# Optimization experiments

Hardware: AMD Instinct MI355X
Metric: run time of the kernel (lower is better)

## Reference

```python
import jax, jax.numpy as jnp
import numpy as np

V, BLK, L, H, C, FF = 50257, 2048, 6, 8, 512, 2048
D = C // H  # head_dim = 64

def setup_inputs() -> dict:
    key = jax.random.key(0)
    ks = jax.random.split(key, 16)
    s = 0.02
    proj_std = 0.02 / np.sqrt(2 * L)
    return {
        'idx': jax.random.randint(ks[0], (2, 2048), 0, V, dtype=jnp.int64),
        'wte': jax.random.normal(ks[1], (V, C), jnp.float32) * s,
        'wpe': jax.random.normal(ks[2], (BLK, C), jnp.float32) * s,
        'ln1_w': jnp.ones((L, C), jnp.float32), 'ln1_b': jnp.zeros((L, C), jnp.float32),
        'c_attn_w': jax.random.normal(ks[3], (L, 3 * C, C), jnp.float32) * s,
        'c_proj_w': jax.random.normal(ks[4], (L, C, C), jnp.float32) * proj_std,
        'ln2_w': jnp.ones((L, C), jnp.float32), 'ln2_b': jnp.zeros((L, C), jnp.float32),
        'fc_w': jax.random.normal(ks[5], (L, FF, C), jnp.float32) * s,
        'proj_w': jax.random.normal(ks[6], (L, C, FF), jnp.float32) * proj_std,
        'lnf_w': jnp.ones((C,), jnp.float32), 'lnf_b': jnp.zeros((C,), jnp.float32),
    }

def _layernorm(x, w, b, eps=1e-5):
    mu = jnp.mean(x, axis=-1, keepdims=True)
    var = jnp.var(x, axis=-1, keepdims=True)
    return (x - mu) * jax.lax.rsqrt(var + eps) * w + b

def _attn(x, attn_w, proj_w, mask):
    B, T, _ = x.shape
    qkv = jnp.einsum('btc,fc->btf', x, attn_w)  # (B,T,3C)
    q, k, v = jnp.split(qkv, 3, axis=-1)
    q = q.reshape(B, T, H, D)
    k = k.reshape(B, T, H, D)
    v = v.reshape(B, T, H, D)
    scale = 1.0 / np.sqrt(D)
    att = jnp.einsum('bthd,bshd->bhts', q, k) * scale  # (B,H,T,T)
    att = jnp.where(mask, att, -jnp.inf)
    att = jax.nn.softmax(att, axis=-1)
    y = jnp.einsum('bhts,bshd->bthd', att, v).reshape(B, T, C)
    return jnp.einsum('btc,oc->bto', y, proj_w)

def reference(idx, wte, wpe, ln1_w, ln1_b, c_attn_w, c_proj_w, ln2_w, ln2_b, fc_w, proj_w, lnf_w, lnf_b):
    B, T = idx.shape
    pos = jnp.arange(T)
    x = wte[idx] + wpe[pos]  # (B,T,C); dropout p=0
    mask = jnp.tril(jnp.ones((T, T), bool))[None, None]
    for i in range(L):
        x = x + _attn(_layernorm(x, ln1_w[i], ln1_b[i]), c_attn_w[i], c_proj_w[i], mask)
        h = _layernorm(x, ln2_w[i], ln2_b[i])
        h = jax.nn.gelu(jnp.einsum('btc,fc->btf', h, fc_w[i]), approximate=False)
        x = x + jnp.einsum('btf,cf->btc', h, proj_w[i])
    x = _layernorm(x, lnf_w, lnf_b)
    logits = jnp.einsum('btc,vc->btv', x, wte)  # tied lm_head
    return logits
```

## Files before the change

### kernel.cpp

```cpp
#include <hip/hip_runtime.h>

typedef unsigned short u16;
typedef short bf16x8 __attribute__((ext_vector_type(8)));
typedef float f32x4 __attribute__((ext_vector_type(4)));
typedef unsigned short u16x4 __attribute__((ext_vector_type(4)));
typedef unsigned short u16x8 __attribute__((ext_vector_type(8)));
typedef unsigned int u32x2 __attribute__((ext_vector_type(2)));

#define B_ 2
#define T_ 2048
#define C_ 512
#define H_ 8
#define FF_ 2048
#define L_ 6
#define V_ 50257
#define M_ (B_*T_)

__device__ __forceinline__ u16 f2b(float f) {
  union { float f; unsigned u; } v; v.f = f;
  unsigned r = v.u + 0x7FFFu + ((v.u >> 16) & 1u);
  return (u16)(r >> 16);
}
__device__ __forceinline__ float b2f(u16 u) {
  union { unsigned u; float f; } v; v.u = ((unsigned)u) << 16; return v.f;
}
__device__ __forceinline__ unsigned pk_bf16(float lo, float hi) {
  unsigned r;
  asm volatile("v_cvt_pk_bf16_f32 %0, %1, %2" : "=v"(r) : "v"(lo), "v"(hi));
  return r;
}
__device__ __forceinline__ float exp2_fast(float x) {
  float r; asm("v_exp_f32 %0, %1" : "=v"(r) : "v"(x)); return r;
}
__device__ __forceinline__ float rcp_fast(float x) {
  float r; asm("v_rcp_f32 %0, %1" : "=v"(r) : "v"(x)); return r;
}

__device__ __forceinline__ void async16(const void* g, void* l) {
  __builtin_amdgcn_global_load_lds((const __attribute__((address_space(1))) unsigned int*)g,
                                   (__attribute__((address_space(3))) unsigned int*)l, 16, 0, 0);
}

template<int N> __device__ __forceinline__ void vwait() {
  if constexpr (N == 0) asm volatile("s_waitcnt vmcnt(0)" ::: "memory");
  else if constexpr (N == 2) asm volatile("s_waitcnt vmcnt(2)" ::: "memory");
  else if constexpr (N == 3) asm volatile("s_waitcnt vmcnt(3)" ::: "memory");
  else if constexpr (N == 4) asm volatile("s_waitcnt vmcnt(4)" ::: "memory");
}

__device__ __forceinline__ bf16x8 scale8(u16x8 v, float s) {
  union { bf16x8 b; unsigned u[4]; } r;
#pragma unroll
  for (int i = 0; i < 4; i++)
    r.u[i] = pk_bf16(b2f(v[2*i]) * s, b2f(v[2*i+1]) * s);
  return r.b;
}

__device__ __forceinline__ float gelu_f(float f) {
  float u = f * f;
  float inner = f * (0.7978845608028654f + 0.03567740814183056f * u);
  inner = fminf(fmaxf(inner, -15.f), 15.f);
  float a = exp2_fast(2.8853900817779268f * inner);
  return f * a * rcp_fast(a + 1.0f);
}

struct CvtArgs { const f32x4* s[5]; u16x4* d[5]; };
__global__ void cvt_all_k(CvtArgs a) {
  const int sizes[5] = { V_*C_/4, L_*3*C_*C_/4, L_*C_*C_/4, L_*FF_*C_/4, L_*C_*FF_/4 };
  int gid = blockIdx.x * blockDim.x + threadIdx.x;
  int stride = gridDim.x * blockDim.x;
#pragma unroll
  for (int seg = 0; seg < 5; seg++) {
    const f32x4* src = a.s[seg];
    u16x4* dst = a.d[seg];
    for (int i = gid; i < sizes[seg]; i += stride) {
      f32x4 v = src[i];
      u16x4 o;
      o[0] = f2b(v[0]); o[1] = f2b(v[1]); o[2] = f2b(v[2]); o[3] = f2b(v[3]);
      dst[i] = o;
    }
  }
}

__global__ void embed_k(const int* __restrict__ idx, const float* __restrict__ wte,
                        const float* __restrict__ wpe, float* __restrict__ x) {
  int t = blockIdx.x * 256 + threadIdx.x;
  int row = t >> 7;
  int c4 = t & 127;
  int tok = idx[row];
  int pos = row & (T_ - 1);
  f32x4 a = ((const f32x4*)(wte + (long)tok * C_))[c4];
  f32x4 p = ((const f32x4*)(wpe + (long)pos * C_))[c4];
  ((f32x4*)x)[t] = a + p;
}

__global__ void ln_k(const float* __restrict__ x, const float* __restrict__ w,
                     const float* __restrict__ b, u16* __restrict__ out) {
  int wv = threadIdx.x >> 6;
  int lane = threadIdx.x & 63;
  int row = blockIdx.x * 4 + wv;
  const f32x4* xr = (const f32x4*)(x + (long)row * C_);
  f32x4 v0 = xr[lane * 2], v1 = xr[lane * 2 + 1];
  float s = 0.f, s2 = 0.f;
#pragma unroll
  for (int j = 0; j < 4; j++) { s += v0[j] + v1[j]; s2 += v0[j]*v0[j] + v1[j]*v1[j]; }
#pragma unroll
  for (int off = 32; off >= 1; off >>= 1) { s += __shfl_xor(s, off); s2 += __shfl_xor(s2, off); }
  float mu = s * (1.f / C_);
  float inv = rsqrtf(s2 * (1.f / C_) - mu * mu + 1e-5f);
  const f32x4* wr = (const f32x4*)w;
  const f32x4* br = (const f32x4*)b;
  f32x4 w0 = wr[lane*2], w1 = wr[lane*2+1], b0 = br[lane*2], b1 = br[lane*2+1];
  u16x8 o;
#pragma unroll
  for (int j = 0; j < 4; j++) {
    o[j]     = f2b((v0[j] - mu) * inv * w0[j] + b0[j]);
    o[j + 4] = f2b((v1[j] - mu) * inv * w1[j] + b1[j]);
  }
  *(u16x8*)(out + (long)row * C_ + lane * 8) = o;
}

template<int EPI, int BM, int BN>
__global__ __launch_bounds__(256) void gemm_bt_k(
    const u16* __restrict__ A, const u16* __restrict__ Bw,
    u16* __restrict__ Cb, float* __restrict__ Cf,
    int N, int K, int ldc)
{
  constexpr int MT = BM / 32;
  constexpr int NT = BN / 32;
  constexpr int AJ = BM / 64;
  constexpr int BJ = BN / 64;
  constexpr int LPT = AJ + BJ;
  __shared__ __align__(16) u16 sA[3][BM * 32];
  __shared__ __align__(16) u16 sB[3][BN * 32];
  const int tid = threadIdx.x;
  const int n0 = blockIdx.x * BN;
  const int m0 = blockIdx.y * BM;
  const int w = tid >> 6;
  const int lane = tid & 63;
  const int wm = (w >> 1) * (BM / 2);
  const int wn = (w & 1) * (BN / 2);
  const int g = lane >> 4;
  const int l15 = lane & 15;
  const int sw3 = l15 & 3;

  f32x4 acc[MT][NT] = {};

  const int nk = K >> 5;
  const int ksw = ((tid & 3) ^ ((tid >> 2) & 3)) * 8;
  const u16* gA[AJ];
  const u16* gB[BJ];
#pragma unroll
  for (int j = 0; j < AJ; j++)
    gA[j] = A + (long)(m0 + (tid >> 2) + j * 64) * K + ksw;
#pragma unroll
  for (int j = 0; j < BJ; j++)
    gB[j] = Bw + (long)(n0 + (tid >> 2) + j * 64) * K + ksw;

  auto stage = [&](int buf, int kt) {
    int ko = kt << 5;
#pragma unroll
    for (int j = 0; j < AJ; j++)
      async16(gA[j] + ko, &sA[buf][(j * 256 + w * 64) * 8]);
#pragma unroll
    for (int j = 0; j < BJ; j++)
      async16(gB[j] + ko, &sB[buf][(j * 256 + w * 64) * 8]);
  };

  stage(0, 0);
  stage(1, 1);
  int cur = 0, nxt = 2;
  for (int kt = 0; kt < nk; kt++) {
    if (kt + 1 < nk) vwait<LPT>(); else vwait<0>();
    __builtin_amdgcn_s_barrier();
    if (kt + 2 < nk) stage(nxt, kt + 2);
    const u16* pa = sA[cur];
    const u16* pb = sB[cur];
    bf16x8 af[MT], bfr[NT];
#pragma unroll
    for (int mt = 0; mt < MT; mt++)
      af[mt] = *(const bf16x8*)(pa + (wm + mt * 16 + l15) * 32 + ((g ^ sw3) * 8));
#pragma unroll
    for (int nt = 0; nt < NT; nt++)
      bfr[nt] = *(const bf16x8*)(pb + (wn + nt * 16 + l15) * 32 + ((g ^ sw3) * 8));
#pragma unroll
    for (int mt = 0; mt < MT; mt++)
#pragma unroll
      for (int nt = 0; nt < NT; nt++)
        acc[mt][nt] = __builtin_amdgcn_mfma_f32_16x16x32_bf16(af[mt], bfr[nt], acc[mt][nt], 0, 0, 0);
    cur = (cur == 2) ? 0 : cur + 1;
    nxt = (nxt == 2) ? 0 : nxt + 1;
  }

#pragma unroll
  for (int mt = 0; mt < MT; mt++) {
    int m = m0 + wm + mt * 16 + g * 4;
#pragma unroll
    for (int nt = 0; nt < NT; nt++) {
      int n = n0 + wn + nt * 16 + l15;
      f32x4 v = acc[mt][nt];
#pragma unroll
      for (int r = 0; r < 4; r++) {
        long ci = (long)(m + r) * ldc + n;
        if (EPI == 0) {
          Cb[ci] = f2b(v[r]);
        } else {
          Cb[ci] = f2b(gelu_f(v[r]));
        }
      }
    }
  }
}

__global__ __launch_bounds__(256) void gemm_bt64_k(
    const u16* __restrict__ A, const u16* __restrict__ Bw,
    float* __restrict__ Cf, int N, int K, int ldc)
{
  __shared__ __align__(16) u16 sA[3][64 * 64];
  __shared__ __align__(16) u16 sB[3][64 * 64];
  const int tid = threadIdx.x;
  const int n0 = blockIdx.x * 64;
  const int m0 = blockIdx.y * 64;
  const int w = tid >> 6;
  const int lane = tid & 63;
  const int wm = (w >> 1) * 32;
  const int wn = (w & 1) * 32;
  const int g = lane >> 4;
  const int l15 = lane & 15;
  const int sw3 = l15 & 3;

  f32x4 acc[2][2] = {};

  const int nk = K >> 6;
  const int srow = tid >> 3;
  const int sl = tid & 7;
  const int kcol = (((sl & 4) | ((sl & 3) ^ (srow & 3)))) * 8;
  const u16* gA[2];
  const u16* gB[2];
#pragma unroll
  for (int j = 0; j < 2; j++) {
    gA[j] = A + (long)(m0 + srow + j * 32) * K + kcol;
    gB[j] = Bw + (long)(n0 + srow + j * 32) * K + kcol;
  }

  auto stage = [&](int buf, int kt) {
    int ko = kt << 6;
#pragma unroll
    for (int j = 0; j < 2; j++)
      async16(gA[j] + ko, &sA[buf][(j * 256 + w * 64) * 8]);
#pragma unroll
    for (int j = 0; j < 2; j++)
      async16(gB[j] + ko, &sB[buf][(j * 256 + w * 64) * 8]);
  };

  stage(0, 0);
  stage(1, 1);
  int cur = 0, nxt = 2;
  for (int kt = 0; kt < nk; kt++) {
    if (kt + 1 < nk) vwait<4>(); else vwait<0>();
    __builtin_amdgcn_s_barrier();
    if (kt + 2 < nk) stage(nxt, kt + 2);
    const u16* pa = sA[cur];
    const u16* pb = sB[cur];
#pragma unroll
    for (int h = 0; h < 2; h++) {
      bf16x8 af[2], bfr[2];
#pragma unroll
      for (int mt = 0; mt < 2; mt++)
        af[mt] = *(const bf16x8*)(pa + (wm + mt * 16 + l15) * 64 + (((g ^ sw3) + h * 4) * 8));
#pragma unroll
      for (int nt = 0; nt < 2; nt++)
        bfr[nt] = *(const bf16x8*)(pb + (wn + nt * 16 + l15) * 64 + (((g ^ sw3) + h * 4) * 8));
#pragma unroll
      for (int mt = 0; mt < 2; mt++)
#pragma unroll
        for (int nt = 0; nt < 2; nt++)
          acc[mt][nt] = __builtin_amdgcn_mfma_f32_16x16x32_bf16(af[mt], bfr[nt], acc[mt][nt], 0, 0, 0);
    }
    cur = (cur == 2) ? 0 : cur + 1;
    nxt = (nxt == 2) ? 0 : nxt + 1;
  }

#pragma unroll
  for (int mt = 0; mt < 2; mt++) {
    int m = m0 + wm + mt * 16 + g * 4;
#pragma unroll
    for (int nt = 0; nt < 2; nt++) {
      int n = n0 + wn + nt * 16 + l15;
      f32x4 v = acc[mt][nt];
#pragma unroll
      for (int r = 0; r < 4; r++)
        Cf[(long)(m + r) * ldc + n] += v[r];
    }
  }
}

__global__ __launch_bounds__(512) void gemm_lmhead_k(
    const u16* __restrict__ A, const u16* __restrict__ Bw,
    float* __restrict__ Cf, int N)
{
  __shared__ __align__(16) u16 sA[3][256 * 32];
  __shared__ __align__(16) u16 sB[3][256 * 32];
  const int K = 512;
  const int bid = blockIdx.x;
  const int swz = (bid & 7) * 394 + (bid >> 3);
  const int m0 = (swz / 197) * 256;
  const int n0 = (swz % 197) * 256;
  const int tid = threadIdx.x;
  const int w = tid >> 6;
  const int lane = tid & 63;
  const int wm = (w >> 1) * 64;
  const int wn = (w & 1) * 128;
  const int g = lane >> 4;
  const int l15 = lane & 15;
  const int swl = (l15 & 3) ^ ((l15 >> 2) & 1);

  f32x4 acc[4][8] = {};

  const int ksw = ((tid & 3) ^ ((tid >> 2) & 3) ^ ((tid >> 4) & 1)) * 8;
  const u16* gA[2];
  const u16* gB[2];
#pragma unroll
  for (int j = 0; j < 2; j++) {
    gA[j] = A + (long)(m0 + (tid >> 2) + j * 128) * K + ksw;
    int brow = n0 + (tid >> 2) + j * 128; if (brow > N - 1) brow = N - 1;
    gB[j] = Bw + (long)brow * K + ksw;
  }

  auto stage = [&](int buf, int kt) {
    int ko = kt << 5;
#pragma unroll
    for (int j = 0; j < 2; j++)
      async16(gA[j] + ko, &sA[buf][(j * 512 + w * 64) * 8]);
#pragma unroll
    for (int j = 0; j < 2; j++)
      async16(gB[j] + ko, &sB[buf][(j * 512 + w * 64) * 8]);
  };

  stage(0, 0);
  stage(1, 1);
  int cur = 0, nxt = 2;
  const int nk = K >> 5;
  for (int kt = 0; kt < nk; kt++) {
    if (kt + 1 < nk) vwait<4>(); else vwait<0>();
    __builtin_amdgcn_s_barrier();
    if (kt + 2 < nk) stage(nxt, kt + 2);
    const u16* pa = sA[cur];
    const u16* pb = sB[cur];
    bf16x8 af[4], bfr[8];
#pragma unroll
    for (int mt = 0; mt < 4; mt++)
      af[mt] = *(const bf16x8*)(pa + (wm + mt * 16 + l15) * 32 + ((g ^ swl) * 8));
#pragma unroll
    for (int nt = 0; nt < 8; nt++)
      bfr[nt] = *(const bf16x8*)(pb + (wn + nt * 16 + l15) * 32 + ((g ^ swl) * 8));
    __builtin_amdgcn_s_setprio(1);
#pragma unroll
    for (int mt = 0; mt < 4; mt++)
#pragma unroll
      for (int nt = 0; nt < 8; nt++)
        acc[mt][nt] = __builtin_amdgcn_mfma_f32_16x16x32_bf16(af[mt], bfr[nt], acc[mt][nt], 0, 0, 0);
    __builtin_amdgcn_s_setprio(0);
    cur = (cur == 2) ? 0 : cur + 1;
    nxt = (nxt == 2) ? 0 : nxt + 1;
  }

#pragma unroll
  for (int mt = 0; mt < 4; mt++) {
    int m = m0 + wm + mt * 16 + g * 4;
#pragma unroll
    for (int nt = 0; nt < 8; nt++) {
      int n = n0 + wn + nt * 16 + l15;
      f32x4 v = acc[mt][nt];
      if (n < N) {
#pragma unroll
        for (int r = 0; r < 4; r++)
          Cf[(long)(m + r) * N + n] = v[r];
      }
    }
  }
}

__global__ __launch_bounds__(256) void attn_k(const u16* __restrict__ qkv, u16* __restrict__ out) {
  const int bh = blockIdx.y;
  const int b = bh >> 3;
  const int h = bh & 7;
  const int tid = threadIdx.x;
  const int wv = tid >> 6;
  const int lane = tid & 63;
  const int g = lane >> 4;
  const int l15 = lane & 15;
  const int qblk = 31 - blockIdx.x;

  __shared__ __align__(16) u16 Ks[2][64 * 64];
  __shared__ __align__(16) u16 Vt[2][64 * 72];
  __shared__ __align__(16) u16 Ps[4][16 * 64];

  const long base = (long)b * T_ * 1536;
  const u16* kbase = qkv + base + 512 + h * 64;
  const u16* vbase = qkv + base + 1024 + h * 64;
  const int kq = tid & 15;
  const int dg = (tid >> 4) & 7;
  const float qscale = 0.18033688011112042f;

  const int q0 = qblk * 64 + wv * 16;

  const u16* qrow = qkv + base + (long)(q0 + l15) * 1536 + h * 64;
  bf16x8 qf0 = scale8(*(const u16x8*)(qrow + g * 8), qscale);
  bf16x8 qf1 = scale8(*(const u16x8*)(qrow + 32 + g * 8), qscale);

  f32x4 o[4] = {};
  float mrun[4] = {-1e30f, -1e30f, -1e30f, -1e30f};
  float lrun[4] = {0.f, 0.f, 0.f, 0.f};
  const int kvend = qblk * 64 + 64;

  u16x8 vreg[4];
#pragma unroll
  for (int i = 0; i < 2; i++) {
    int chunk = i * 256 + tid;
    int row = chunk >> 3, c8 = chunk & 7;
    async16(kbase + (long)row * 1536 + (c8 ^ (row & 7)) * 8,
            &Ks[0][(i * 256 + wv * 64) * 8]);
  }
  if (tid < 128) {
#pragma unroll
    for (int t = 0; t < 4; t++)
      vreg[t] = *(const u16x8*)(vbase + (long)(kq + 16 * t) * 1536 + dg * 8);
#pragma unroll
    for (int e = 0; e < 8; e++) {
      int d = dg * 8 + e;
      u32x2 wq = { (unsigned)vreg[0][e] | ((unsigned)vreg[1][e] << 16),
                   (unsigned)vreg[2][e] | ((unsigned)vreg[3][e] << 16) };
      *(u32x2*)(&Vt[0][d * 72 + kq * 4]) = wq;
    }
  }
  __syncthreads();

  int cur = 0;
  for (int j0 = 0; j0 < kvend; j0 += 64, cur ^= 1) {
    const bool more = (j0 + 64) < kvend;
    if (more) {
      int jn = j0 + 64;
#pragma unroll
      for (int i = 0; i < 2; i++) {
        int chunk = i * 256 + tid;
        int row = chunk >> 3, c8 = chunk & 7;
        async16(kbase + (long)(jn + row) * 1536 + (c8 ^ (row & 7)) * 8,
                &Ks[cur ^ 1][(i * 256 + wv * 64) * 8]);
      }
      if (tid < 128) {
#pragma unroll
        for (int t = 0; t < 4; t++)
          vreg[t] = *(const u16x8*)(vbase + (long)(jn + kq + 16 * t) * 1536 + dg * 8);
      }
    }

    f32x4 s[4] = {};
    const u16* kp = Ks[cur];
#pragma unroll
    for (int t = 0; t < 4; t++) {
      int row = t * 16 + l15;
      const u16* kr = kp + row * 64;
      bf16x8 k0 = *(const bf16x8*)(kr + ((g ^ (row & 7)) * 8));
      bf16x8 k1 = *(const bf16x8*)(kr + (((4 + g) ^ (row & 7)) * 8));
      s[t] = __builtin_amdgcn_mfma_f32_16x16x32_bf16(qf0, k0, s[t], 0, 0, 0);
      s[t] = __builtin_amdgcn_mfma_f32_16x16x32_bf16(qf1, k1, s[t], 0, 0, 0);
    }

    const bool diag = (j0 + 64) == kvend;
    u16* pw = Ps[wv];
#pragma unroll
    for (int r = 0; r < 4; r++) {
      int row = q0 + g * 4 + r;
      float v0 = s[0][r], v1 = s[1][r], v2 = s[2][r], v3 = s[3][r];
      if (diag) {
        if (j0 +      l15 > row) v0 = -1e30f;
        if (j0 + 16 + l15 > row) v1 = -1e30f;
        if (j0 + 32 + l15 > row) v2 = -1e30f;
        if (j0 + 48 + l15 > row) v3 = -1e30f;
      }
      float mloc = fmaxf(fmaxf(v0, v1), fmaxf(v2, v3));
      float m = mrun[r];
      if (!__all(mloc <= m + 8.0f)) {
        float mx = mloc;
        mx = fmaxf(mx, __shfl_xor(mx, 1));
        mx = fmaxf(mx, __shfl_xor(mx, 2));
        mx = fmaxf(mx, __shfl_xor(mx, 4));
        mx = fmaxf(mx, __shfl_xor(mx, 8));
        float mn = fmaxf(m, mx);
        float sc2 = exp2_fast(m - mn);
        lrun[r] *= sc2;
#pragma unroll
        for (int dt = 0; dt < 4; dt++) o[dt][r] *= sc2;
        m = mn; mrun[r] = mn;
      }
      float e0 = exp2_fast(v0 - m), e1 = exp2_fast(v1 - m);
      float e2 = exp2_fast(v2 - m), e3 = exp2_fast(v3 - m);
      lrun[r] += (e0 + e1) + (e2 + e3);
      u32x2 pkq = { pk_bf16(e0, e1), pk_bf16(e2, e3) };
      int prow = g * 4 + r;
      int byt = prow * 128 + ((((l15 >> 1) ^ (prow & 7)) << 4)) + (l15 & 1) * 8;
      *(u32x2*)((char*)pw + byt) = pkq;
    }

    const u16* vt = Vt[cur];
    bf16x8 pf0 = *(const bf16x8*)((char*)pw + l15 * 128 + (((g) ^ (l15 & 7)) << 4));
    bf16x8 pf1 = *(const bf16x8*)((char*)pw + l15 * 128 + (((4 + g) ^ (l15 & 7)) << 4));
#pragma unroll
    for (int dt = 0; dt < 4; dt++) {
      int d = dt * 16 + l15;
      bf16x8 vf0 = *(const bf16x8*)(vt + d * 72 + g * 8);
      bf16x8 vf1 = *(const bf16x8*)(vt + d * 72 + 32 + g * 8);
      o[dt] = __builtin_amdgcn_mfma_f32_16x16x32_bf16(pf0, vf0, o[dt], 0, 0, 0);
      o[dt] = __builtin_amdgcn_mfma_f32_16x16x32_bf16(pf1, vf1, o[dt], 0, 0, 0);
    }

    if (more && tid < 128) {
#pragma unroll
      for (int e = 0; e < 8; e++) {
        int d = dg * 8 + e;
        u32x2 wq = { (unsigned)vreg[0][e] | ((unsigned)vreg[1][e] << 16),
                     (unsigned)vreg[2][e] | ((unsigned)vreg[3][e] << 16) };
        *(u32x2*)(&Vt[cur ^ 1][d * 72 + kq * 4]) = wq;
      }
    }
    __syncthreads();
  }

#pragma unroll
  for (int r = 0; r < 4; r++) {
    float ls = lrun[r];
    ls += __shfl_xor(ls, 1); ls += __shfl_xor(ls, 2);
    ls += __shfl_xor(ls, 4); ls += __shfl_xor(ls, 8);
    float inv = 1.0f / ls;
    int row = q0 + g * 4 + r;
    u16* orow = out + (long)(b * T_ + row) * C_ + h * 64;
#pragma unroll
    for (int dt = 0; dt < 4; dt++)
      orow[dt * 16 + l15] = f2b(o[dt][r] * inv);
  }
}

extern "C" void kernel_launch(void* const* d_in, const int* in_sizes, int n_in,
                              void* d_out, int out_size, void* d_ws, size_t ws_size,
                              hipStream_t stream) {
  const int*   idx    = (const int*)  d_in[0];
  const float* wte    = (const float*)d_in[1];
  const float* wpe    = (const float*)d_in[2];
  const float* ln1w   = (const float*)d_in[3];
  const float* ln1b   = (const float*)d_in[4];
  const float* wattn  = (const float*)d_in[5];
  const float* wcproj = (const float*)d_in[6];
  const float* ln2w   = (const float*)d_in[7];
  const float* ln2b   = (const float*)d_in[8];
  const float* wfc    = (const float*)d_in[9];
  const float* wproj2 = (const float*)d_in[10];
  const float* lnfw   = (const float*)d_in[11];
  const float* lnfb   = (const float*)d_in[12];
  float* out = (float*)d_out;

  char* p = (char*)d_ws;
  size_t off = 0;
  auto alloc = [&](size_t bytes) -> void* {
    void* r = p + off; off += (bytes + 255) & ~(size_t)255; return r;
  };
  float* x    = (float*)alloc((size_t)M_ * C_ * 4);
  u16* xn     = (u16*)alloc((size_t)M_ * C_ * 2);
  u16* qkvb   = (u16*)alloc((size_t)M_ * 3 * C_ * 2);
  u16* attb   = (u16*)alloc((size_t)M_ * C_ * 2);
  u16* hb     = (u16*)alloc((size_t)M_ * FF_ * 2);
  u16* wteB   = (u16*)alloc((size_t)V_ * C_ * 2);
  u16* wattnB = (u16*)alloc((size_t)L_ * 3 * C_ * C_ * 2);
  u16* wprojB = (u16*)alloc((size_t)L_ * C_ * C_ * 2);
  u16* wfcB   = (u16*)alloc((size_t)L_ * FF_ * C_ * 2);
  u16* wp2B   = (u16*)alloc((size_t)L_ * C_ * FF_ * 2);
  if (off > ws_size) return;

  CvtArgs ca;
  ca.s[0] = (const f32x4*)wte;    ca.d[0] = (u16x4*)wteB;
  ca.s[1] = (const f32x4*)wattn;  ca.d[1] = (u16x4*)wattnB;
  ca.s[2] = (const f32x4*)wcproj; ca.d[2] = (u16x4*)wprojB;
  ca.s[3] = (const f32x4*)wfc;    ca.d[3] = (u16x4*)wfcB;
  ca.s[4] = (const f32x4*)wproj2; ca.d[4] = (u16x4*)wp2B;
  cvt_all_k<<<dim3(2048), dim3(256), 0, stream>>>(ca);

  embed_k<<<dim3(M_ * C_ / 4 / 256), dim3(256), 0, stream>>>(idx, wte, wpe, x);

  for (int l = 0; l < L_; l++) {
    ln_k<<<dim3(M_ / 4), dim3(256), 0, stream>>>(x, ln1w + l * C_, ln1b + l * C_, xn);
    gemm_bt_k<0, 64, 128><<<dim3(12, 64), dim3(256), 0, stream>>>(
        xn, wattnB + (size_t)l * 3 * C_ * C_, qkvb, nullptr, 3 * C_, C_, 3 * C_);
    attn_k<<<dim3(32, B_ * H_), dim3(256), 0, stream>>>(qkvb, attb);
    gemm_bt64_k<<<dim3(8, 64), dim3(256), 0, stream>>>(
        attb, wprojB + (size_t)l * C_ * C_, x, C_, C_, C_);
    ln_k<<<dim3(M_ / 4), dim3(256), 0, stream>>>(x, ln2w + l * C_, ln2b + l * C_, xn);
    gemm_bt_k<2, 128, 128><<<dim3(16, 32), dim3(256), 0, stream>>>(
        xn, wfcB + (size_t)l * FF_ * C_, hb, nullptr, FF_, C_, FF_);
    gemm_bt64_k<<<dim3(8, 64), dim3(256), 0, stream>>>(
        hb, wp2B + (size_t)l * C_ * FF_, x, C_, FF_, C_);
  }
  ln_k<<<dim3(M_ / 4), dim3(256), 0, stream>>>(x, lnfw, lnfb, xn);
  gemm_lmhead_k<<<dim3(16 * 197), dim3(512), 0, stream>>>(xn, wteB, out, V_);
}
```

Baseline: 1.258 ms.

## Remap GEMM block indices per XCD and shrink LM-head N tile to 128

All GEMMs now use a 1-D grid whose block IDs are decoded so that each of the 8 XCDs (selected by bid&7) owns a contiguous band of M rows. The intent is to keep the A tiles shared within one XCD's L2 instead of scattering them across dies. The LM-head kernel also shrinks its N tile from 256 to 128, halving its accumulators and B shared memory. That raises block count and occupancy but reloads the A rows twice as often.

Measured after the change: 1.219 ms. -3.1%, faster.

```diff
diff --git a/kernel.cpp b/kernel.cpp
--- a/kernel.cpp
+++ b/kernel.cpp
@@ -131,11 +131,15 @@
   constexpr int AJ = BM / 64;
   constexpr int BJ = BN / 64;
   constexpr int LPT = AJ + BJ;
+  constexpr int MX = (M_ / BM) / 8;
   __shared__ __align__(16) u16 sA[3][BM * 32];
   __shared__ __align__(16) u16 sB[3][BN * 32];
+  const int bid = blockIdx.x;
+  const int xc = bid & 7;
+  const int jj = bid >> 3;
+  const int m0 = (xc * MX + (jj % MX)) * BM;
+  const int n0 = (jj / MX) * BN;
   const int tid = threadIdx.x;
-  const int n0 = blockIdx.x * BN;
-  const int m0 = blockIdx.y * BM;
   const int w = tid >> 6;
   const int lane = tid & 63;
   const int wm = (w >> 1) * (BM / 2);
@@ -218,9 +222,12 @@
 {
   __shared__ __align__(16) u16 sA[3][64 * 64];
   __shared__ __align__(16) u16 sB[3][64 * 64];
+  const int bid = blockIdx.x;
+  const int xc = bid & 7;
+  const int jj = bid >> 3;
+  const int m0 = (xc * 8 + (jj & 7)) * 64;
+  const int n0 = (jj >> 3) * 64;
   const int tid = threadIdx.x;
-  const int n0 = blockIdx.x * 64;
-  const int m0 = blockIdx.y * 64;
   const int w = tid >> 6;
   const int lane = tid & 63;
   const int wm = (w >> 1) * 32;
@@ -300,41 +307,40 @@
     float* __restrict__ Cf, int N)
 {
   __shared__ __align__(16) u16 sA[3][256 * 32];
-  __shared__ __align__(16) u16 sB[3][256 * 32];
+  __shared__ __align__(16) u16 sB[3][128 * 32];
   const int K = 512;
   const int bid = blockIdx.x;
-  const int swz = (bid & 7) * 394 + (bid >> 3);
-  const int m0 = (swz / 197) * 256;
-  const int n0 = (swz % 197) * 256;
+  const int xc = bid & 7;
+  const int j = bid >> 3;
+  const int half = (j >= 393);
+  const int jn = half ? j - 393 : j;
+  const int m0 = (xc * 2 + half) * 256;
+  const int n0 = jn * 128;
   const int tid = threadIdx.x;
   const int w = tid >> 6;
   const int lane = tid & 63;
   const int wm = (w >> 1) * 64;
-  const int wn = (w & 1) * 128;
+  const int wn = (w & 1) * 64;
   const int g = lane >> 4;
   const int l15 = lane & 15;
   const int swl = (l15 & 3) ^ ((l15 >> 2) & 1);
 
-  f32x4 acc[4][8] = {};
+  f32x4 acc[4][4] = {};
 
   const int ksw = ((tid & 3) ^ ((tid >> 2) & 3) ^ ((tid >> 4) & 1)) * 8;
   const u16* gA[2];
-  const u16* gB[2];
-#pragma unroll
-  for (int j = 0; j < 2; j++) {
-    gA[j] = A + (long)(m0 + (tid >> 2) + j * 128) * K + ksw;
-    int brow = n0 + (tid >> 2) + j * 128; if (brow > N - 1) brow = N - 1;
-    gB[j] = Bw + (long)brow * K + ksw;
-  }
+#pragma unroll
+  for (int jA = 0; jA < 2; jA++)
+    gA[jA] = A + (long)(m0 + (tid >> 2) + jA * 128) * K + ksw;
+  int brow = n0 + (tid >> 2); if (brow > N - 1) brow = N - 1;
+  const u16* gB0 = Bw + (long)brow * K + ksw;
 
   auto stage = [&](int buf, int kt) {
     int ko = kt << 5;
 #pragma unroll
-    for (int j = 0; j < 2; j++)
-      async16(gA[j] + ko, &sA[buf][(j * 512 + w * 64) * 8]);
-#pragma unroll
-    for (int j = 0; j < 2; j++)
-      async16(gB[j] + ko, &sB[buf][(j * 512 + w * 64) * 8]);
+    for (int jA = 0; jA < 2; jA++)
+      async16(gA[jA] + ko, &sA[buf][(jA * 512 + w * 64) * 8]);
+    async16(gB0 + ko, &sB[buf][(w * 64) * 8]);
   };
 
   stage(0, 0);
@@ -342,23 +348,23 @@
   int cur = 0, nxt = 2;
   const int nk = K >> 5;
   for (int kt = 0; kt < nk; kt++) {
-    if (kt + 1 < nk) vwait<4>(); else vwait<0>();
+    if (kt + 1 < nk) vwait<3>(); else vwait<0>();
     __builtin_amdgcn_s_barrier();
     if (kt + 2 < nk) stage(nxt, kt + 2);
     const u16* pa = sA[cur];
     const u16* pb = sB[cur];
-    bf16x8 af[4], bfr[8];
+    bf16x8 af[4], bfr[4];
 #pragma unroll
     for (int mt = 0; mt < 4; mt++)
       af[mt] = *(const bf16x8*)(pa + (wm + mt * 16 + l15) * 32 + ((g ^ swl) * 8));
 #pragma unroll
-    for (int nt = 0; nt < 8; nt++)
+    for (int nt = 0; nt < 4; nt++)
       bfr[nt] = *(const bf16x8*)(pb + (wn + nt * 16 + l15) * 32 + ((g ^ swl) * 8));
     __builtin_amdgcn_s_setprio(1);
 #pragma unroll
     for (int mt = 0; mt < 4; mt++)
 #pragma unroll
-      for (int nt = 0; nt < 8; nt++)
+      for (int nt = 0; nt < 4; nt++)
         acc[mt][nt] = __builtin_amdgcn_mfma_f32_16x16x32_bf16(af[mt], bfr[nt], acc[mt][nt], 0, 0, 0);
     __builtin_amdgcn_s_setprio(0);
     cur = (cur == 2) ? 0 : cur + 1;
@@ -369,7 +375,7 @@
   for (int mt = 0; mt < 4; mt++) {
     int m = m0 + wm + mt * 16 + g * 4;
 #pragma unroll
-    for (int nt = 0; nt < 8; nt++) {
+    for (int nt = 0; nt < 4; nt++) {
       int n = n0 + wn + nt * 16 + l15;
       f32x4 v = acc[mt][nt];
       if (n < N) {
@@ -588,17 +594,17 @@
 
   for (int l = 0; l < L_; l++) {
     ln_k<<<dim3(M_ / 4), dim3(256), 0, stream>>>(x, ln1w + l * C_, ln1b + l * C_, xn);
-    gemm_bt_k<0, 64, 128><<<dim3(12, 64), dim3(256), 0, stream>>>(
+    gemm_bt_k<0, 64, 128><<<dim3(768), dim3(256), 0, stream>>>(
         xn, wattnB + (size_t)l * 3 * C_ * C_, qkvb, nullptr, 3 * C_, C_, 3 * C_);
     attn_k<<<dim3(32, B_ * H_), dim3(256), 0, stream>>>(qkvb, attb);
-    gemm_bt64_k<<<dim3(8, 64), dim3(256), 0, stream>>>(
+    gemm_bt64_k<<<dim3(512), dim3(256), 0, stream>>>(
         attb, wprojB + (size_t)l * C_ * C_, x, C_, C_, C_);
     ln_k<<<dim3(M_ / 4), dim3(256), 0, stream>>>(x, ln2w + l * C_, ln2b + l * C_, xn);
-    gemm_bt_k<2, 128, 128><<<dim3(16, 32), dim3(256), 0, stream>>>(
+    gemm_bt_k<2, 128, 128><<<dim3(512), dim3(256), 0, stream>>>(
         xn, wfcB + (size_t)l * FF_ * C_, hb, nullptr, FF_, C_, FF_);
-    gemm_bt64_k<<<dim3(8, 64), dim3(256), 0, stream>>>(
+    gemm_bt64_k<<<dim3(512), dim3(256), 0, stream>>>(
         hb, wp2B + (size_t)l * C_ * FF_, x, C_, FF_, C_);
   }
   ln_k<<<dim3(M_ / 4), dim3(256), 0, stream>>>(x, lnfw, lnfb, xn);
-  gemm_lmhead_k<<<dim3(16 * 197), dim3(512), 0, stream>>>(xn, wteB, out, V_);
-}
+  gemm_lmhead_k<<<dim3(8 * 786), dim3(512), 0, stream>>>(xn, wteB, out, V_);
+}
```
